# Kernel optimization log

Hardware: AMD Instinct MI355X
Metric: run time of the kernel (lower is better)

The kernel has to match this reference:

```python
import jax, jax.numpy as jnp
import numpy as np

H, W = 2048, 4096
NUM_FRAMES, NUM_CAMERAS = 200, 4


def setup_inputs() -> dict:
    key = jax.random.key(0)
    k0, k1, k2, k3, k4 = jax.random.split(key, 5)
    exposure_params = 0.1 * jax.random.normal(k0, (NUM_FRAMES,), dtype=jnp.float32)
    vignetting_params = 0.05 * jax.random.normal(k1, (NUM_CAMERAS, 3, 5), dtype=jnp.float32)
    color_params = 0.05 * jax.random.normal(k2, (NUM_FRAMES, 8), dtype=jnp.float32)
    crf_params = 0.1 * jax.random.normal(k3, (NUM_CAMERAS, 3, 4), dtype=jnp.float32)
    rgb_in = jax.random.uniform(k4, (H, W, 3), dtype=jnp.float32)
    xs = jnp.arange(W, dtype=jnp.float32) + 0.5  # pixel-center x
    ys = jnp.arange(H, dtype=jnp.float32) + 0.5  # pixel-center y
    gx, gy = jnp.meshgrid(xs, ys)  # each [H, W]
    pixel_coords = jnp.stack([gx, gy], axis=-1)  # [H, W, 2] (x, y)
    return {
        'exposure_params': exposure_params,
        'vignetting_params': vignetting_params,
        'color_params': color_params,
        'crf_params': crf_params,
        'rgb_in': rgb_in,
        'pixel_coords': pixel_coords,
        'resolution_w': W,
        'resolution_h': H,
        'camera_idx': 1,
        'frame_idx': 3,
    }


def _ppisp_forward(exposure_params, vignetting_params, color_params, crf_params,
                   rgb_flat, coords_flat, resolution_w, resolution_h,
                   camera_idx, frame_idx):
    # rgb_flat: [N, 3], coords_flat: [N, 2]
    rgb = rgb_flat
    # --- stage 1: per-frame exposure scale ---
    if frame_idx >= 0:
        rgb = rgb * jnp.exp(exposure_params[frame_idx])
    # --- stage 2: per-camera radial vignetting polynomial (per channel) ---
    if camera_idx >= 0:
        vp = vignetting_params[camera_idx]  # [3, 5] = (cx, cy, a1, a2, a3) per channel
        cx = (0.5 + vp[:, 0]) * resolution_w   # [3] optical center x in pixels
        cy = (0.5 + vp[:, 1]) * resolution_h   # [3]
        norm2 = (0.5 * resolution_w) ** 2 + (0.5 * resolution_h) ** 2
        dx = coords_flat[:, :1] - cx           # [N, 3]
        dy = coords_flat[:, 1:] - cy           # [N, 3]
        r2 = (dx * dx + dy * dy) / norm2       # normalized squared radius
        vig = 1.0 + r2 * (vp[:, 2] + r2 * (vp[:, 3] + r2 * vp[:, 4]))  # Horner cubic in r^2
        rgb = rgb * vig
    # --- stage 3: per-frame 8-param color correction (identity-anchored 3x3) ---
    if frame_idx >= 0:
        p = color_params[frame_idx]  # [8]
        one = jnp.ones((), dtype=p.dtype)
        M = jnp.stack([
            jnp.stack([one + p[0], p[1], p[2]]),
            jnp.stack([p[3], one + p[4], p[5]]),
            jnp.stack([p[6], p[7], one]),
        ])  # [3, 3]
        rgb = rgb @ M.T
    # --- stage 4: per-camera CRF gamma curve (per channel, 4 params) ---
    if camera_idx >= 0:
        q = crf_params[camera_idx]      # [3, 4] = (log_gamma, b1, b2, b3)
        gamma = jnp.exp(q[:, 0])        # [3]
        x = jnp.clip(rgb, 0.0, 1.0)
        y = x ** gamma
        # smooth perturbation anchored at y=0 and y=1
        y = y + y * (1.0 - y) * (q[:, 1] + q[:, 2] * y + q[:, 3] * (1.0 - y))
        rgb = y
    return rgb


def reference(exposure_params, vignetting_params, color_params, crf_params,
              rgb_in, pixel_coords, resolution_w, resolution_h, camera_idx, frame_idx):
    original_shape = rgb_in.shape
    rgb_flat = rgb_in.reshape(-1, 3).astype(jnp.float32)
    coords_flat = pixel_coords.reshape(-1, 2).astype(jnp.float32)
    out = _ppisp_forward(exposure_params.astype(jnp.float32),
                         vignetting_params.astype(jnp.float32),
                         color_params.astype(jnp.float32),
                         crf_params.astype(jnp.float32),
                         rgb_flat, coords_flat,
                         int(resolution_w), int(resolution_h),
                         int(camera_idx), int(frame_idx))
    return out.reshape(original_shape)
```

## Files before the change

### kernel.cpp

```cpp
#include <hip/hip_runtime.h>
#include <math.h>

constexpr int W = 4096;
constexpr int H = 2048;
constexpr int W_SHIFT = 12;
constexpr int NPIX = W * H;
constexpr int NFLOAT = NPIX * 3;
constexpr int BLOCK = 256;
constexpr int PIX_PER_THREAD = 8;
constexpr int FLT_PER_THREAD = 3 * PIX_PER_THREAD;
constexpr int FLT_PER_BLOCK = BLOCK * FLT_PER_THREAD;
constexpr int FLT_PER_WAVE = 64 * FLT_PER_THREAD;
constexpr int GRID = NFLOAT / FLT_PER_BLOCK;

#define AS1 __attribute__((address_space(1)))
#define AS3 __attribute__((address_space(3)))

__global__ __launch_bounds__(BLOCK) void ppisp_kernel(
    const float* __restrict__ exposure,
    const float* __restrict__ vigp,
    const float* __restrict__ colorp,
    const float* __restrict__ crfp,
    const float* __restrict__ rgb_in,
    const int*   __restrict__ cam_idx,
    const int*   __restrict__ frm_idx,
    float*       __restrict__ out)
{
    __shared__ float smem[FLT_PER_BLOCK];

    const int t    = threadIdx.x;
    const int wave = t >> 6;
    const int lane = t & 63;

    {
        const float* gw = rgb_in + (size_t)blockIdx.x * FLT_PER_BLOCK
                                 + wave * FLT_PER_WAVE;
        #pragma unroll
        for (int j = 0; j < 6; ++j) {
            const float* g = gw + j * 256 + lane * 4;
            const float* l = &smem[wave * FLT_PER_WAVE + j * 256 + lane * 4];
            __builtin_amdgcn_global_load_lds((const AS1 void*)g, (AS3 void*)l,
                                             16, 0, 0);
        }
    }

    const int cam = __builtin_amdgcn_readfirstlane(cam_idx[0]);
    const int frm = __builtin_amdgcn_readfirstlane(frm_idx[0]);

    const float escale = (frm >= 0) ? __expf(exposure[frm]) : 1.0f;

    float cx[3], cy[3], a1[3], a2[3], a3[3];
    if (cam >= 0) {
        const float* vp = vigp + cam * 15;
        #pragma unroll
        for (int c = 0; c < 3; ++c) {
            cx[c] = (0.5f + vp[c * 5 + 0]) * (float)W;
            cy[c] = (0.5f + vp[c * 5 + 1]) * (float)H;
            a1[c] = vp[c * 5 + 2];
            a2[c] = vp[c * 5 + 3];
            a3[c] = vp[c * 5 + 4];
        }
    } else {
        #pragma unroll
        for (int c = 0; c < 3; ++c) {
            cx[c] = cy[c] = 0.0f;
            a1[c] = a2[c] = a3[c] = 0.0f;
        }
    }
    const float nx = 0.5f * (float)W, ny = 0.5f * (float)H;
    const float inv_norm2 = 1.0f / (nx * nx + ny * ny);

    float M[9];
    if (frm >= 0) {
        const float* p = colorp + frm * 8;
        M[0] = 1.0f + p[0]; M[1] = p[1];        M[2] = p[2];
        M[3] = p[3];        M[4] = 1.0f + p[4]; M[5] = p[5];
        M[6] = p[6];        M[7] = p[7];        M[8] = 1.0f;
    } else {
        M[0] = 1.0f; M[1] = 0.0f; M[2] = 0.0f;
        M[3] = 0.0f; M[4] = 1.0f; M[5] = 0.0f;
        M[6] = 0.0f; M[7] = 0.0f; M[8] = 1.0f;
    }

    float gam[3], b1[3], b2[3], b3[3];
    const int crf_on = (cam >= 0);
    if (crf_on) {
        const float* q = crfp + cam * 12;
        #pragma unroll
        for (int c = 0; c < 3; ++c) {
            gam[c] = __expf(q[c * 4 + 0]);
            b1[c]  = q[c * 4 + 1];
            b2[c]  = q[c * 4 + 2];
            b3[c]  = q[c * 4 + 3];
        }
    } else {
        #pragma unroll
        for (int c = 0; c < 3; ++c) { gam[c] = 1.0f; b1[c] = b2[c] = b3[c] = 0.0f; }
    }

    __syncthreads();

    float4* s4 = (float4*)smem;
    float v[FLT_PER_THREAD];
    #pragma unroll
    for (int j = 0; j < 6; ++j) {
        const float4 x = s4[t * 6 + j];
        v[4 * j + 0] = x.x; v[4 * j + 1] = x.y;
        v[4 * j + 2] = x.z; v[4 * j + 3] = x.w;
    }

    const int p0 = blockIdx.x * (FLT_PER_BLOCK / 3) + t * PIX_PER_THREAD;
    #pragma unroll
    for (int k = 0; k < PIX_PER_THREAD; ++k) {
        const int p = p0 + k;
        const float px = (float)(p & (W - 1)) + 0.5f;
        const float py = (float)(p >> W_SHIFT) + 0.5f;

        float ch[3];
        #pragma unroll
        for (int c = 0; c < 3; ++c) ch[c] = v[k * 3 + c] * escale;

        #pragma unroll
        for (int c = 0; c < 3; ++c) {
            const float dx = px - cx[c];
            const float dy = py - cy[c];
            const float r2 = (dx * dx + dy * dy) * inv_norm2;
            ch[c] *= 1.0f + r2 * (a1[c] + r2 * (a2[c] + r2 * a3[c]));
        }

        float o[3];
        o[0] = M[0] * ch[0] + M[1] * ch[1] + M[2] * ch[2];
        o[1] = M[3] * ch[0] + M[4] * ch[1] + M[5] * ch[2];
        o[2] = M[6] * ch[0] + M[7] * ch[1] + M[8] * ch[2];

        if (crf_on) {
            #pragma unroll
            for (int c = 0; c < 3; ++c) {
                const float x = fminf(fmaxf(o[c], 0.0f), 1.0f);
                float y = exp2f(gam[c] * __log2f(x));
                y = y + y * (1.0f - y) * (b1[c] + b2[c] * y + b3[c] * (1.0f - y));
                o[c] = y;
            }
        }

        v[k * 3 + 0] = o[0];
        v[k * 3 + 1] = o[1];
        v[k * 3 + 2] = o[2];
    }

    #pragma unroll
    for (int j = 0; j < 6; ++j)
        s4[t * 6 + j] = make_float4(v[4 * j + 0], v[4 * j + 1],
                                    v[4 * j + 2], v[4 * j + 3]);

    __syncthreads();

    {
        float4* out4 = (float4*)out + (size_t)blockIdx.x * (FLT_PER_BLOCK / 4);
        const int base = wave * (FLT_PER_WAVE / 4);
        #pragma unroll
        for (int j = 0; j < 6; ++j) {
            const int idx = base + j * 64 + lane;
            out4[idx] = s4[idx];
        }
    }
}

extern "C" void kernel_launch(void* const* d_in, const int* in_sizes, int n_in,
                              void* d_out, int out_size, void* d_ws, size_t ws_size,
                              hipStream_t stream) {
    const float* exposure = (const float*)d_in[0];
    const float* vigp     = (const float*)d_in[1];
    const float* colorp   = (const float*)d_in[2];
    const float* crfp     = (const float*)d_in[3];
    const float* rgb_in   = (const float*)d_in[4];
    const int* cam_idx = (const int*)d_in[8];
    const int* frm_idx = (const int*)d_in[9];
    float* out = (float*)d_out;

    ppisp_kernel<<<dim3(GRID), dim3(BLOCK), 0, stream>>>(
        exposure, vigp, colorp, crfp, rgb_in, cam_idx, frm_idx, out);
}
```

Baseline: 225.7 us.

## Replace LDS-staged coalesced transfers with direct per-thread float4 global loads/stores

Removes the shared-memory staging (global_load_lds into LDS, barriers, LDS read-back and LDS-to-global copy) and has each thread load and store its own 24 contiguous floats directly as six float4 accesses. This drops the LDS traffic, the two __syncthreads and the 24 KB shared allocation, which may raise occupancy. In exchange each wave's accesses become strided (96-byte stride between lanes per instruction), so coalescing per instruction is worse and relies on caches to merge the lines.

```diff
diff --git a/kernel.cpp b/kernel.cpp
--- a/kernel.cpp
+++ b/kernel.cpp
@@ -10,11 +10,7 @@
 constexpr int PIX_PER_THREAD = 8;
 constexpr int FLT_PER_THREAD = 3 * PIX_PER_THREAD;
 constexpr int FLT_PER_BLOCK = BLOCK * FLT_PER_THREAD;
-constexpr int FLT_PER_WAVE = 64 * FLT_PER_THREAD;
 constexpr int GRID = NFLOAT / FLT_PER_BLOCK;
-
-#define AS1 __attribute__((address_space(1)))
-#define AS3 __attribute__((address_space(3)))
 
 __global__ __launch_bounds__(BLOCK) void ppisp_kernel(
     const float* __restrict__ exposure,
@@ -26,23 +22,14 @@
     const int*   __restrict__ frm_idx,
     float*       __restrict__ out)
 {
-    __shared__ float smem[FLT_PER_BLOCK];
+    const int t = threadIdx.x;
+    const size_t base = (size_t)blockIdx.x * FLT_PER_BLOCK
+                      + (size_t)t * FLT_PER_THREAD;
 
-    const int t    = threadIdx.x;
-    const int wave = t >> 6;
-    const int lane = t & 63;
-
-    {
-        const float* gw = rgb_in + (size_t)blockIdx.x * FLT_PER_BLOCK
-                                 + wave * FLT_PER_WAVE;
-        #pragma unroll
-        for (int j = 0; j < 6; ++j) {
-            const float* g = gw + j * 256 + lane * 4;
-            const float* l = &smem[wave * FLT_PER_WAVE + j * 256 + lane * 4];
-            __builtin_amdgcn_global_load_lds((const AS1 void*)g, (AS3 void*)l,
-                                             16, 0, 0);
-        }
-    }
+    const float4* __restrict__ g4 = (const float4*)(rgb_in + base);
+    float4 r[6];
+    #pragma unroll
+    for (int j = 0; j < 6; ++j) r[j] = g4[j];
 
     const int cam = __builtin_amdgcn_readfirstlane(cam_idx[0]);
     const int frm = __builtin_amdgcn_readfirstlane(frm_idx[0]);
@@ -98,15 +85,11 @@
         for (int c = 0; c < 3; ++c) { gam[c] = 1.0f; b1[c] = b2[c] = b3[c] = 0.0f; }
     }
 
-    __syncthreads();
-
-    float4* s4 = (float4*)smem;
     float v[FLT_PER_THREAD];
     #pragma unroll
     for (int j = 0; j < 6; ++j) {
-        const float4 x = s4[t * 6 + j];
-        v[4 * j + 0] = x.x; v[4 * j + 1] = x.y;
-        v[4 * j + 2] = x.z; v[4 * j + 3] = x.w;
+        v[4 * j + 0] = r[j].x; v[4 * j + 1] = r[j].y;
+        v[4 * j + 2] = r[j].z; v[4 * j + 3] = r[j].w;
     }
 
     const int p0 = blockIdx.x * (FLT_PER_BLOCK / 3) + t * PIX_PER_THREAD;
@@ -148,22 +131,11 @@
         v[k * 3 + 2] = o[2];
     }
 
+    float4* __restrict__ o4 = (float4*)(out + base);
     #pragma unroll
     for (int j = 0; j < 6; ++j)
-        s4[t * 6 + j] = make_float4(v[4 * j + 0], v[4 * j + 1],
-                                    v[4 * j + 2], v[4 * j + 3]);
-
-    __syncthreads();
-
-    {
-        float4* out4 = (float4*)out + (size_t)blockIdx.x * (FLT_PER_BLOCK / 4);
-        const int base = wave * (FLT_PER_WAVE / 4);
-        #pragma unroll
-        for (int j = 0; j < 6; ++j) {
-            const int idx = base + j * 64 + lane;
-            out4[idx] = s4[idx];
-        }
-    }
+        o4[j] = make_float4(v[4 * j + 0], v[4 * j + 1],
+                            v[4 * j + 2], v[4 * j + 3]);
 }
 
 extern "C" void kernel_launch(void* const* d_in, const int* in_sizes, int n_in,
```

New measurement: 233.9 us. 3.6% more time.

## Double-buffer per-wave LDS chunks with async global-to-LDS prefetch loop

Applied to the files above, without the earlier changes.

Replaces the single-shot block (load everything into LDS, barrier, compute, barrier, store) with a per-wave loop over four chunks of 64×4 pixels. Each wave owns two LDS buffers and prefetches the next chunk with global_load_lds while it computes and stores the current one. Explicit vmcnt waits replace the block-wide __syncthreads. The grid shrinks to 2048 blocks. The goal is to overlap load latency with compute and stores and to remove barrier stalls. The cost is hand-counted vmcnt values that assume gfx9 counting of stores, plus fewer resident pixels per wave at any one time.

```diff
diff --git a/kernel.cpp b/kernel.cpp
--- a/kernel.cpp
+++ b/kernel.cpp
@@ -7,11 +7,14 @@
 constexpr int NPIX = W * H;
 constexpr int NFLOAT = NPIX * 3;
 constexpr int BLOCK = 256;
-constexpr int PIX_PER_THREAD = 8;
-constexpr int FLT_PER_THREAD = 3 * PIX_PER_THREAD;
-constexpr int FLT_PER_BLOCK = BLOCK * FLT_PER_THREAD;
-constexpr int FLT_PER_WAVE = 64 * FLT_PER_THREAD;
-constexpr int GRID = NFLOAT / FLT_PER_BLOCK;
+constexpr int WAVES = BLOCK / 64;
+constexpr int PIX_PER_LANE = 4;
+constexpr int FLT_PER_LANE = 3 * PIX_PER_LANE;
+constexpr int CHUNK_FLT = 64 * FLT_PER_LANE;
+constexpr int CHUNK_PIX = CHUNK_FLT / 3;
+constexpr int CHUNKS = NFLOAT / CHUNK_FLT;
+constexpr int GRID = 2048;
+constexpr int C = CHUNKS / (GRID * WAVES);
 
 #define AS1 __attribute__((address_space(1)))
 #define AS3 __attribute__((address_space(3)))
@@ -26,23 +29,13 @@
     const int*   __restrict__ frm_idx,
     float*       __restrict__ out)
 {
-    __shared__ float smem[FLT_PER_BLOCK];
+    __shared__ float smem[WAVES][2][CHUNK_FLT];
 
     const int t    = threadIdx.x;
     const int wave = t >> 6;
     const int lane = t & 63;
 
-    {
-        const float* gw = rgb_in + (size_t)blockIdx.x * FLT_PER_BLOCK
-                                 + wave * FLT_PER_WAVE;
-        #pragma unroll
-        for (int j = 0; j < 6; ++j) {
-            const float* g = gw + j * 256 + lane * 4;
-            const float* l = &smem[wave * FLT_PER_WAVE + j * 256 + lane * 4];
-            __builtin_amdgcn_global_load_lds((const AS1 void*)g, (AS3 void*)l,
-                                             16, 0, 0);
-        }
-    }
+    const int wc0 = blockIdx.x * (WAVES * C) + wave * C;
 
     const int cam = __builtin_amdgcn_readfirstlane(cam_idx[0]);
     const int frm = __builtin_amdgcn_readfirstlane(frm_idx[0]);
@@ -98,70 +91,98 @@
         for (int c = 0; c < 3; ++c) { gam[c] = 1.0f; b1[c] = b2[c] = b3[c] = 0.0f; }
     }
 
-    __syncthreads();
-
-    float4* s4 = (float4*)smem;
-    float v[FLT_PER_THREAD];
+    asm volatile("s_waitcnt vmcnt(0)" ::: "memory");
+
+    {
+        const size_t f0 = (size_t)wc0 * CHUNK_FLT;
+        #pragma unroll
+        for (int j = 0; j < 3; ++j) {
+            __builtin_amdgcn_global_load_lds(
+                (const AS1 void*)(rgb_in + f0 + j * 256 + lane * 4),
+                (AS3 void*)&smem[wave][0][j * 256], 16, 0, 0);
+        }
+    }
+
     #pragma unroll
-    for (int j = 0; j < 6; ++j) {
-        const float4 x = s4[t * 6 + j];
-        v[4 * j + 0] = x.x; v[4 * j + 1] = x.y;
-        v[4 * j + 2] = x.z; v[4 * j + 3] = x.w;
-    }
-
-    const int p0 = blockIdx.x * (FLT_PER_BLOCK / 3) + t * PIX_PER_THREAD;
-    #pragma unroll
-    for (int k = 0; k < PIX_PER_THREAD; ++k) {
-        const int p = p0 + k;
-        const float px = (float)(p & (W - 1)) + 0.5f;
-        const float py = (float)(p >> W_SHIFT) + 0.5f;
-
-        float ch[3];
-        #pragma unroll
-        for (int c = 0; c < 3; ++c) ch[c] = v[k * 3 + c] * escale;
-
-        #pragma unroll
-        for (int c = 0; c < 3; ++c) {
-            const float dx = px - cx[c];
-            const float dy = py - cy[c];
-            const float r2 = (dx * dx + dy * dy) * inv_norm2;
-            ch[c] *= 1.0f + r2 * (a1[c] + r2 * (a2[c] + r2 * a3[c]));
-        }
-
-        float o[3];
-        o[0] = M[0] * ch[0] + M[1] * ch[1] + M[2] * ch[2];
-        o[1] = M[3] * ch[0] + M[4] * ch[1] + M[5] * ch[2];
-        o[2] = M[6] * ch[0] + M[7] * ch[1] + M[8] * ch[2];
-
-        if (crf_on) {
+    for (int i = 0; i < C; ++i) {
+        const int cbuf = i & 1;
+
+        if (i + 1 < C) {
+            const size_t fn = (size_t)(wc0 + i + 1) * CHUNK_FLT;
+            #pragma unroll
+            for (int j = 0; j < 3; ++j) {
+                __builtin_amdgcn_global_load_lds(
+                    (const AS1 void*)(rgb_in + fn + j * 256 + lane * 4),
+                    (AS3 void*)&smem[wave][cbuf ^ 1][j * 256], 16, 0, 0);
+            }
+        }
+
+        if (i == 0 || i == C - 1) {
+            asm volatile("s_waitcnt vmcnt(3)" ::: "memory");
+        } else {
+            asm volatile("s_waitcnt vmcnt(6)" ::: "memory");
+        }
+        __builtin_amdgcn_sched_barrier(0);
+
+        float4* sb = (float4*)smem[wave][cbuf];
+        const float4 x0 = sb[lane * 3 + 0];
+        const float4 x1 = sb[lane * 3 + 1];
+        const float4 x2 = sb[lane * 3 + 2];
+
+        float v[FLT_PER_LANE];
+        v[0] = x0.x; v[1]  = x0.y; v[2]  = x0.z; v[3]  = x0.w;
+        v[4] = x1.x; v[5]  = x1.y; v[6]  = x1.z; v[7]  = x1.w;
+        v[8] = x2.x; v[9]  = x2.y; v[10] = x2.z; v[11] = x2.w;
+
+        const int pb = (wc0 + i) * CHUNK_PIX + lane * PIX_PER_LANE;
+        #pragma unroll
+        for (int k = 0; k < PIX_PER_LANE; ++k) {
+            const int p = pb + k;
+            const float px = (float)(p & (W - 1)) + 0.5f;
+            const float py = (float)(p >> W_SHIFT) + 0.5f;
+
+            float ch[3];
+            #pragma unroll
+            for (int c = 0; c < 3; ++c) ch[c] = v[k * 3 + c] * escale;
+
             #pragma unroll
             for (int c = 0; c < 3; ++c) {
-                const float x = fminf(fmaxf(o[c], 0.0f), 1.0f);
-                float y = exp2f(gam[c] * __log2f(x));
-                y = y + y * (1.0f - y) * (b1[c] + b2[c] * y + b3[c] * (1.0f - y));
-                o[c] = y;
+                const float dx = px - cx[c];
+                const float dy = py - cy[c];
+                const float r2 = (dx * dx + dy * dy) * inv_norm2;
+                ch[c] *= 1.0f + r2 * (a1[c] + r2 * (a2[c] + r2 * a3[c]));
             }
-        }
-
-        v[k * 3 + 0] = o[0];
-        v[k * 3 + 1] = o[1];
-        v[k * 3 + 2] = o[2];
-    }
-
-    #pragma unroll
-    for (int j = 0; j < 6; ++j)
-        s4[t * 6 + j] = make_float4(v[4 * j + 0], v[4 * j + 1],
-                                    v[4 * j + 2], v[4 * j + 3]);
-
-    __syncthreads();
-
-    {
-        float4* out4 = (float4*)out + (size_t)blockIdx.x * (FLT_PER_BLOCK / 4);
-        const int base = wave * (FLT_PER_WAVE / 4);
-        #pragma unroll
-        for (int j = 0; j < 6; ++j) {
-            const int idx = base + j * 64 + lane;
-            out4[idx] = s4[idx];
+
+            float o[3];
+            o[0] = M[0] * ch[0] + M[1] * ch[1] + M[2] * ch[2];
+            o[1] = M[3] * ch[0] + M[4] * ch[1] + M[5] * ch[2];
+            o[2] = M[6] * ch[0] + M[7] * ch[1] + M[8] * ch[2];
+
+            if (crf_on) {
+                #pragma unroll
+                for (int c = 0; c < 3; ++c) {
+                    const float x = fminf(fmaxf(o[c], 0.0f), 1.0f);
+                    float y = exp2f(gam[c] * __log2f(x));
+                    y = y + y * (1.0f - y) * (b1[c] + b2[c] * y + b3[c] * (1.0f - y));
+                    o[c] = y;
+                }
+            }
+
+            v[k * 3 + 0] = o[0];
+            v[k * 3 + 1] = o[1];
+            v[k * 3 + 2] = o[2];
+        }
+
+        sb[lane * 3 + 0] = make_float4(v[0], v[1], v[2],  v[3]);
+        sb[lane * 3 + 1] = make_float4(v[4], v[5], v[6],  v[7]);
+        sb[lane * 3 + 2] = make_float4(v[8], v[9], v[10], v[11]);
+
+        {
+            const float4* sl = (const float4*)smem[wave][cbuf];
+            float4* og = (float4*)(out + (size_t)(wc0 + i) * CHUNK_FLT);
+            #pragma unroll
+            for (int j = 0; j < 3; ++j)
+                og[j * 64 + lane] = sl[j * 64 + lane];
         }
     }
 }
```

Result: no change. 229.6 us (+1.7%).
